# Optimization experiments

Measured on AMD Instinct MI355X. Metric: run time of the kernel, lower is better.

The kernel has to match this reference:

```python
import jax, jax.numpy as jnp
import numpy as np


def _binarize_ste(w):
    # forward: sign(w) in {-1, +1}; backward: identity (straight-through)
    wb = jnp.where(w >= 0, 1.0, -1.0).astype(w.dtype)
    return w + jax.lax.stop_gradient(wb - w)


def setup_inputs() -> dict:
    key = jax.random.key(0)
    k1, k2 = jax.random.split(key)
    IN, OUT, N = 2048, 2048, 8192
    x = jax.random.normal(k1, (N, IN), dtype=jnp.float32)
    # kaiming_uniform-like init: U(-bound, bound), bound = sqrt(6/in)*? (gain sqrt(5) default in torch)
    bound = float(np.sqrt(6.0 / IN))
    weight = jax.random.uniform(k2, (OUT, IN), dtype=jnp.float32, minval=-bound, maxval=bound)
    bias = jnp.zeros((OUT,), dtype=jnp.float32)
    return {"x": x, "weight": weight, "bias": bias}


def reference(x, weight, bias):
    w_binary = _binarize_ste(weight)  # [out, in], values in {-1, +1}
    # F.linear: x @ W^T + b
    return jnp.einsum('ni,oi->no', x, w_binary) + bias
```

## Files before the change

kernel.cpp:

```cpp
#include <hip/hip_runtime.h>
#include <stdint.h>


typedef __bf16 bf16x8 __attribute__((ext_vector_type(8)));
typedef float f32x4 __attribute__((ext_vector_type(4)));

typedef const __attribute__((address_space(1))) void* gas_ptr;
typedef __attribute__((address_space(3))) void* lds_ptr;

__device__ __forceinline__ unsigned short f2bf_rne(float f) {
    unsigned int u = __builtin_bit_cast(unsigned int, f);
    u += 0x7fffu + ((u >> 16) & 1u);
    return (unsigned short)(u >> 16);
}

__global__ __launch_bounds__(256) void prep_kernel(
    const float* __restrict__ x, const float* __restrict__ w,
    unsigned short* __restrict__ xb, unsigned short* __restrict__ wb,
    int nx8, int nxB, int nw4)
{
    const int b = blockIdx.x;
    if (b < nxB) {
        int i = b * 256 + threadIdx.x;
        if (i >= nx8) return;
        const float4* p = reinterpret_cast<const float4*>(x + (size_t)i * 8);
        float4 f0 = p[0], f1 = p[1];
        union { unsigned short s[8]; uint4 v; } o;
        o.s[0] = f2bf_rne(f0.x); o.s[1] = f2bf_rne(f0.y);
        o.s[2] = f2bf_rne(f0.z); o.s[3] = f2bf_rne(f0.w);
        o.s[4] = f2bf_rne(f1.x); o.s[5] = f2bf_rne(f1.y);
        o.s[6] = f2bf_rne(f1.z); o.s[7] = f2bf_rne(f1.w);
        *reinterpret_cast<uint4*>(xb + (size_t)i * 8) = o.v;
    } else {
        int i = (b - nxB) * 256 + threadIdx.x;
        if (i >= nw4) return;
        float4 f = reinterpret_cast<const float4*>(w)[i];
        union { unsigned short s[4]; uint2 v; } o;
        o.s[0] = (f.x >= 0.f) ? 0x3F80u : 0xBF80u;
        o.s[1] = (f.y >= 0.f) ? 0x3F80u : 0xBF80u;
        o.s[2] = (f.z >= 0.f) ? 0x3F80u : 0xBF80u;
        o.s[3] = (f.w >= 0.f) ? 0x3F80u : 0xBF80u;
        reinterpret_cast<uint2*>(wb)[i] = o.v;
    }
}

#define WAITLGKM0 asm volatile("s_waitcnt lgkmcnt(0)")
#define WAITLGKM8 asm volatile("s_waitcnt lgkmcnt(8)")
#define WAITVM0   asm volatile("s_waitcnt vmcnt(0)")
#define SBAR      __builtin_amdgcn_s_barrier()
#define SCHEDB    __builtin_amdgcn_sched_barrier(0)

__global__ __launch_bounds__(512, 2) void gemm_bin_kernel(
    const unsigned short* __restrict__ A,
    const unsigned short* __restrict__ B,
    const float* __restrict__ bias,
    float* __restrict__ C,
    int M, int N, int K)
{
    __shared__ __align__(16) unsigned char smem_raw[131072];
    unsigned short* const sm = (unsigned short*)smem_raw;

    const int tid  = threadIdx.x;
    const int lane = tid & 63;
    const int wave = tid >> 6;
    const int wm   = wave >> 2;
    const int wn   = wave & 3;
    const int bm   = blockIdx.y;
    const int bn   = blockIdx.x;

    const unsigned short* __restrict__ Agb = A + (size_t)(bm * 256) * K;
    const unsigned short* __restrict__ Bgb = B + (size_t)(bn * 256) * K;

    const int r15 = lane & 15;
    const int kc  = lane >> 4;
    const int sw  = ((r15 >> 2) & 1) << 1;

    const int baseA0 = wm * 8192 + r15 * 64 + ((kc    ) ^ sw) * 8;
    const int baseA1 = wm * 8192 + r15 * 64 + ((kc + 4) ^ sw) * 8;
    const int bBq    = 16384 + (wn >> 1) * 8192 + (wn & 1) * 4096 + r15 * 64;
    const int baseB0 = bBq + ((kc    ) ^ sw) * 8;
    const int baseB1 = bBq + ((kc + 4) ^ sw) * 8;

    int gsoff[2], ldoff[2];
#pragma unroll
    for (int j = 0; j < 2; ++j) {
        const int g  = j * 512 + tid;
        const int rl = g >> 3;
        const int c  = (g & 7) ^ (((rl >> 2) & 1) << 1);
        gsoff[j] = rl * K + c * 8;
        ldoff[j] = g * 8;
    }

    const int colb = bn * 256 + wn * 64;
    float bv[4];
#pragma unroll
    for (int nf = 0; nf < 4; ++nf) {
        bv[nf] = bias[colb + nf * 16 + r15];
        asm volatile("" :: "v"(bv[nf]));
    }

    f32x4 acc[8][4];
#pragma unroll
    for (int m = 0; m < 8; ++m)
#pragma unroll
        for (int n = 0; n < 4; ++n)
#pragma unroll
            for (int r = 0; r < 4; ++r) acc[m][n][r] = 0.f;

    bf16x8 bfr[4][2];

    auto stage2 = [&](const unsigned short* gsrc, unsigned short* dst) {
#pragma unroll
        for (int j = 0; j < 2; ++j)
            __builtin_amdgcn_global_load_lds((gas_ptr)(gsrc + gsoff[j]),
                                             (lds_ptr)(dst + ldoff[j]), 16, 0, 0);
    };

    const int KT = K >> 6;

    stage2(Agb,                   sm);
    stage2(Agb + (size_t)128 * K, sm + 8192);
    stage2(Bgb,                   sm + 16384);
    stage2(Bgb + (size_t)128 * K, sm + 24576);
    WAITVM0;
    SBAR;
    SCHEDB;
    asm volatile("" ::: "memory");

    for (int T = 0; T < KT; ++T) {
        const unsigned short* bb = sm + (T & 1) * 32768;
        unsigned short* nb = sm + ((T + 1) & 1) * 32768;
        const int pf = (T + 1 < KT);
        const unsigned short* gaN = Agb + (size_t)(T + 1) * 64;
        const unsigned short* gbN = Bgb + (size_t)(T + 1) * 64;

#pragma unroll
        for (int mh = 0; mh < 4; ++mh) {
            if (mh == 0) {
#pragma unroll
                for (int nf = 0; nf < 4; ++nf) {
                    bfr[nf][0] = *reinterpret_cast<const bf16x8*>(bb + baseB0 + nf * 1024);
                    bfr[nf][1] = *reinterpret_cast<const bf16x8*>(bb + baseB1 + nf * 1024);
                }
            }
            bf16x8 af[2][2];
#pragma unroll
            for (int mi = 0; mi < 2; ++mi) {
                af[mi][0] = *reinterpret_cast<const bf16x8*>(bb + baseA0 + (mh * 2 + mi) * 1024);
                af[mi][1] = *reinterpret_cast<const bf16x8*>(bb + baseA1 + (mh * 2 + mi) * 1024);
            }
            if (mh == 0 && pf) {
                stage2(gaN,                   nb);
                stage2(gaN + (size_t)128 * K, nb + 8192);
            }
            if (mh == 1 && pf) {
                stage2(gbN,                   nb + 16384);
                stage2(gbN + (size_t)128 * K, nb + 24576);
            }
            if (mh == 0) WAITLGKM8;
            SBAR;
            WAITLGKM0;
            __builtin_amdgcn_s_setprio(1);
#pragma unroll
            for (int kk = 0; kk < 2; ++kk)
#pragma unroll
                for (int mi = 0; mi < 2; ++mi)
#pragma unroll
                    for (int nf = 0; nf < 4; ++nf)
                        acc[mh * 2 + mi][nf] = __builtin_amdgcn_mfma_f32_16x16x32_bf16(
                            af[mi][kk], bfr[nf][kk], acc[mh * 2 + mi][nf], 0, 0, 0);
            __builtin_amdgcn_s_setprio(0);
            if (mh == 3) WAITVM0;
            SBAR;
            if (mh == 3) {
                SCHEDB;
                asm volatile("" ::: "memory");
            }
        }
    }

    const int row0 = bm * 256 + wm * 128 + kc * 4;
#pragma unroll
    for (int mf = 0; mf < 8; ++mf)
#pragma unroll
        for (int nf = 0; nf < 4; ++nf) {
            float* cp = C + (size_t)(row0 + mf * 16) * N + colb + nf * 16 + r15;
#pragma unroll
            for (int r = 0; r < 4; ++r)
                cp[(size_t)r * N] = acc[mf][nf][r] + bv[nf];
        }
}

extern "C" void kernel_launch(void* const* d_in, const int* in_sizes, int n_in,
                              void* d_out, int out_size, void* d_ws, size_t ws_size,
                              hipStream_t stream) {
    const float* x    = (const float*)d_in[0];
    const float* w    = (const float*)d_in[1];
    const float* bias = (const float*)d_in[2];
    float* out = (float*)d_out;

    const int K = 2048;
    const int N = in_sizes[2];
    const int M = in_sizes[0] / K;

    unsigned short* xb = (unsigned short*)d_ws;
    unsigned short* wb = xb + (size_t)M * K;

    const int nx8 = (M * K) / 8;
    const int nw4 = (N * K) / 4;
    const int nxB = (nx8 + 255) / 256;
    const int nwB = (nw4 + 255) / 256;
    prep_kernel<<<nxB + nwB, 256, 0, stream>>>(x, w, xb, wb, nx8, nxB, nw4);

    dim3 grid(N / 256, M / 256);
    gemm_bin_kernel<<<grid, 512, 0, stream>>>(xb, wb, bias, out, M, N, K);
}
```

Before: 191.3 us.

## Pack binarized weights into bitmasks and expand to bf16 in registers

The prep kernel now packs the signs of the weights into one bit each, laid out per 64-wide K tile. The GEMM loads these bits straight into registers and expands them into bf16 ±1 MFMA operands, so weight tiles no longer pass through LDS. The A tile moves to a 3-slot LDS ring with deeper prefetch, using split vmcnt waits. This cuts weight bandwidth and LDS traffic and lowers LDS use, but adds ALU work for the bit expansion and uncoalesced 8-byte global loads per lane.

```diff
diff --git a/kernel.cpp b/kernel.cpp
--- a/kernel.cpp
+++ b/kernel.cpp
@@ -16,8 +16,8 @@
 
 __global__ __launch_bounds__(256) void prep_kernel(
     const float* __restrict__ x, const float* __restrict__ w,
-    unsigned short* __restrict__ xb, unsigned short* __restrict__ wb,
-    int nx8, int nxB, int nw4)
+    unsigned short* __restrict__ xb, unsigned char* __restrict__ wbits,
+    int nx8, int nxB, int nw8, int K)
 {
     const int b = blockIdx.x;
     if (b < nxB) {
@@ -33,31 +33,39 @@
         *reinterpret_cast<uint4*>(xb + (size_t)i * 8) = o.v;
     } else {
         int i = (b - nxB) * 256 + threadIdx.x;
-        if (i >= nw4) return;
-        float4 f = reinterpret_cast<const float4*>(w)[i];
-        union { unsigned short s[4]; uint2 v; } o;
-        o.s[0] = (f.x >= 0.f) ? 0x3F80u : 0xBF80u;
-        o.s[1] = (f.y >= 0.f) ? 0x3F80u : 0xBF80u;
-        o.s[2] = (f.z >= 0.f) ? 0x3F80u : 0xBF80u;
-        o.s[3] = (f.w >= 0.f) ? 0x3F80u : 0xBF80u;
-        reinterpret_cast<uint2*>(wb)[i] = o.v;
+        if (i >= nw8) return;
+        const int kt = i >> 14;
+        const int n  = (i >> 3) & 2047;
+        const int kb = i & 7;
+        const float4* p = reinterpret_cast<const float4*>(
+            w + (size_t)n * K + kt * 64 + kb * 8);
+        float4 f0 = p[0], f1 = p[1];
+        unsigned bt = 0;
+        bt |= (f0.x >= 0.f) ? 0u : 1u;
+        bt |= (f0.y >= 0.f) ? 0u : 2u;
+        bt |= (f0.z >= 0.f) ? 0u : 4u;
+        bt |= (f0.w >= 0.f) ? 0u : 8u;
+        bt |= (f1.x >= 0.f) ? 0u : 16u;
+        bt |= (f1.y >= 0.f) ? 0u : 32u;
+        bt |= (f1.z >= 0.f) ? 0u : 64u;
+        bt |= (f1.w >= 0.f) ? 0u : 128u;
+        wbits[i] = (unsigned char)bt;
     }
 }
 
 #define WAITLGKM0 asm volatile("s_waitcnt lgkmcnt(0)")
-#define WAITLGKM8 asm volatile("s_waitcnt lgkmcnt(8)")
-#define WAITVM0   asm volatile("s_waitcnt vmcnt(0)")
+#define WAITVM8   asm volatile("s_waitcnt vmcnt(8)")
+#define WAITVM4   asm volatile("s_waitcnt vmcnt(4)")
 #define SBAR      __builtin_amdgcn_s_barrier()
-#define SCHEDB    __builtin_amdgcn_sched_barrier(0)
 
 __global__ __launch_bounds__(512, 2) void gemm_bin_kernel(
     const unsigned short* __restrict__ A,
-    const unsigned short* __restrict__ B,
+    const unsigned char*  __restrict__ Wb,
     const float* __restrict__ bias,
     float* __restrict__ C,
     int M, int N, int K)
 {
-    __shared__ __align__(16) unsigned char smem_raw[131072];
+    __shared__ __align__(16) unsigned char smem_raw[98304];
     unsigned short* const sm = (unsigned short*)smem_raw;
 
     const int tid  = threadIdx.x;
@@ -69,7 +77,6 @@
     const int bn   = blockIdx.x;
 
     const unsigned short* __restrict__ Agb = A + (size_t)(bm * 256) * K;
-    const unsigned short* __restrict__ Bgb = B + (size_t)(bn * 256) * K;
 
     const int r15 = lane & 15;
     const int kc  = lane >> 4;
@@ -77,13 +84,10 @@
 
     const int baseA0 = wm * 8192 + r15 * 64 + ((kc    ) ^ sw) * 8;
     const int baseA1 = wm * 8192 + r15 * 64 + ((kc + 4) ^ sw) * 8;
-    const int bBq    = 16384 + (wn >> 1) * 8192 + (wn & 1) * 4096 + r15 * 64;
-    const int baseB0 = bBq + ((kc    ) ^ sw) * 8;
-    const int baseB1 = bBq + ((kc + 4) ^ sw) * 8;
-
-    int gsoff[2], ldoff[2];
-#pragma unroll
-    for (int j = 0; j < 2; ++j) {
+
+    int gsoff[4], ldoff[4];
+#pragma unroll
+    for (int j = 0; j < 4; ++j) {
         const int g  = j * 512 + tid;
         const int rl = g >> 3;
         const int c  = (g & 7) ^ (((rl >> 2) & 1) << 1);
@@ -107,57 +111,63 @@
 #pragma unroll
             for (int r = 0; r < 4; ++r) acc[m][n][r] = 0.f;
 
+    uint2 bitsCur[4], bitsNxt[4];
     bf16x8 bfr[4][2];
-
-    auto stage2 = [&](const unsigned short* gsrc, unsigned short* dst) {
-#pragma unroll
-        for (int j = 0; j < 2; ++j)
-            __builtin_amdgcn_global_load_lds((gas_ptr)(gsrc + gsoff[j]),
-                                             (lds_ptr)(dst + ldoff[j]), 16, 0, 0);
+    const int shb = kc * 8;
+
+    auto loadbits = [&](int kt, uint2* dst) {
+        const unsigned char* base = Wb + (size_t)kt * ((size_t)N * 8);
+#pragma unroll
+        for (int nf = 0; nf < 4; ++nf)
+            dst[nf] = *reinterpret_cast<const uint2*>(
+                base + (size_t)(colb + nf * 16 + r15) * 8);
     };
+    auto stageA = [&](int T, int slot) {
+        unsigned short* d = sm + slot * 16384;
+        const unsigned short* g = Agb + (size_t)T * 64;
+#pragma unroll
+        for (int j = 0; j < 4; ++j)
+            __builtin_amdgcn_global_load_lds((gas_ptr)(g + gsoff[j]),
+                                             (lds_ptr)(d + ldoff[j]), 16, 0, 0);
+    };
+    auto expand = [&]() {
+#pragma unroll
+        for (int nf = 0; nf < 4; ++nf)
+#pragma unroll
+            for (int kk = 0; kk < 2; ++kk) {
+                unsigned w32 = kk ? bitsCur[nf].y : bitsCur[nf].x;
+                unsigned bbits = (w32 >> shb) & 0xffu;
+                union { unsigned u[4]; bf16x8 v; } o;
+                o.u[0] = 0x3F803F80u | ((bbits &   1u) << 15) | ((bbits &   2u) << 30);
+                o.u[1] = 0x3F803F80u | ((bbits &   4u) << 13) | ((bbits &   8u) << 28);
+                o.u[2] = 0x3F803F80u | ((bbits &  16u) << 11) | ((bbits &  32u) << 26);
+                o.u[3] = 0x3F803F80u | ((bbits &  64u) <<  9) | ((bbits & 128u) << 24);
+                bfr[nf][kk] = o.v;
+            }
+    };
 
     const int KT = K >> 6;
 
-    stage2(Agb,                   sm);
-    stage2(Agb + (size_t)128 * K, sm + 8192);
-    stage2(Bgb,                   sm + 16384);
-    stage2(Bgb + (size_t)128 * K, sm + 24576);
-    WAITVM0;
+    loadbits(0, bitsCur);
+    stageA(0, 0);
+    stageA(1, 1);
+    WAITVM4;
     SBAR;
-    SCHEDB;
-    asm volatile("" ::: "memory");
-
+
+    int sc = 0, sp = 2;
     for (int T = 0; T < KT; ++T) {
-        const unsigned short* bb = sm + (T & 1) * 32768;
-        unsigned short* nb = sm + ((T + 1) & 1) * 32768;
-        const int pf = (T + 1 < KT);
-        const unsigned short* gaN = Agb + (size_t)(T + 1) * 64;
-        const unsigned short* gbN = Bgb + (size_t)(T + 1) * 64;
-
+        const unsigned short* bb = sm + sc * 16384;
 #pragma unroll
         for (int mh = 0; mh < 4; ++mh) {
-            if (mh == 0) {
-#pragma unroll
-                for (int nf = 0; nf < 4; ++nf) {
-                    bfr[nf][0] = *reinterpret_cast<const bf16x8*>(bb + baseB0 + nf * 1024);
-                    bfr[nf][1] = *reinterpret_cast<const bf16x8*>(bb + baseB1 + nf * 1024);
-                }
-            }
+            if (mh == 0) expand();
             bf16x8 af[2][2];
 #pragma unroll
             for (int mi = 0; mi < 2; ++mi) {
                 af[mi][0] = *reinterpret_cast<const bf16x8*>(bb + baseA0 + (mh * 2 + mi) * 1024);
                 af[mi][1] = *reinterpret_cast<const bf16x8*>(bb + baseA1 + (mh * 2 + mi) * 1024);
             }
-            if (mh == 0 && pf) {
-                stage2(gaN,                   nb);
-                stage2(gaN + (size_t)128 * K, nb + 8192);
-            }
-            if (mh == 1 && pf) {
-                stage2(gbN,                   nb + 16384);
-                stage2(gbN + (size_t)128 * K, nb + 24576);
-            }
-            if (mh == 0) WAITLGKM8;
+            if (mh == 0 && T + 1 < KT) loadbits(T + 1, bitsNxt);
+            if (mh == 1 && T + 2 < KT) stageA(T + 2, sp);
             SBAR;
             WAITLGKM0;
             __builtin_amdgcn_s_setprio(1);
@@ -170,13 +180,16 @@
                         acc[mh * 2 + mi][nf] = __builtin_amdgcn_mfma_f32_16x16x32_bf16(
                             af[mi][kk], bfr[nf][kk], acc[mh * 2 + mi][nf], 0, 0, 0);
             __builtin_amdgcn_s_setprio(0);
-            if (mh == 3) WAITVM0;
+            if (mh == 3) {
+                if (T < KT - 2)       { WAITVM8; }
+                else if (T == KT - 2) { WAITVM4; }
+            }
             SBAR;
-            if (mh == 3) {
-                SCHEDB;
-                asm volatile("" ::: "memory");
-            }
         }
+#pragma unroll
+        for (int nf = 0; nf < 4; ++nf) bitsCur[nf] = bitsNxt[nf];
+        sc = (sc == 2) ? 0 : sc + 1;
+        sp = (sp == 2) ? 0 : sp + 1;
     }
 
     const int row0 = bm * 256 + wm * 128 + kc * 4;
@@ -204,14 +217,14 @@
     const int M = in_sizes[0] / K;
 
     unsigned short* xb = (unsigned short*)d_ws;
-    unsigned short* wb = xb + (size_t)M * K;
+    unsigned char* wbits = (unsigned char*)(xb + (size_t)M * K);
 
     const int nx8 = (M * K) / 8;
-    const int nw4 = (N * K) / 4;
+    const int nw8 = (N * K) / 8;
     const int nxB = (nx8 + 255) / 256;
-    const int nwB = (nw4 + 255) / 256;
-    prep_kernel<<<nxB + nwB, 256, 0, stream>>>(x, w, xb, wb, nx8, nxB, nw4);
+    const int nwB = (nw8 + 255) / 256;
+    prep_kernel<<<nxB + nwB, 256, 0, stream>>>(x, w, xb, wbits, nx8, nxB, nw8, K);
 
     dim3 grid(N / 256, M / 256);
-    gemm_bin_kernel<<<grid, 512, 0, stream>>>(xb, wb, bias, out, M, N, K);
-}
+    gemm_bin_kernel<<<grid, 512, 0, stream>>>(xb, wbits, bias, out, M, N, K);
+}
```

Measured after the change: 207.1 us. 8.2% more time.

## Restructure GEMM main loop into 4-stage K=32 pipeline with prefetch depth two

Applied to the files above, without the earlier changes.

Replaces the double-buffered K=64 tile loop with a four-slot ring of K=32 stages, prefetching two stages ahead and waiting with vmcnt(4) so global loads stay in flight across iterations. The LDS layout changes to 32-element rows with a new XOR swizzle, and A/B staging is split across two half-steps of MFMA work. This aims to hide global-to-LDS latency better, at the cost of more barriers per K element and possible new LDS bank conflicts.

```diff
diff --git a/kernel.cpp b/kernel.cpp
--- a/kernel.cpp
+++ b/kernel.cpp
@@ -45,10 +45,9 @@
 }
 
 #define WAITLGKM0 asm volatile("s_waitcnt lgkmcnt(0)")
-#define WAITLGKM8 asm volatile("s_waitcnt lgkmcnt(8)")
+#define WAITVM4   asm volatile("s_waitcnt vmcnt(4)")
 #define WAITVM0   asm volatile("s_waitcnt vmcnt(0)")
 #define SBAR      __builtin_amdgcn_s_barrier()
-#define SCHEDB    __builtin_amdgcn_sched_barrier(0)
 
 __global__ __launch_bounds__(512, 2) void gemm_bin_kernel(
     const unsigned short* __restrict__ A,
@@ -73,20 +72,27 @@
 
     const int r15 = lane & 15;
     const int kc  = lane >> 4;
-    const int sw  = ((r15 >> 2) & 1) << 1;
-
-    const int baseA0 = wm * 8192 + r15 * 64 + ((kc    ) ^ sw) * 8;
-    const int baseA1 = wm * 8192 + r15 * 64 + ((kc + 4) ^ sw) * 8;
-    const int bBq    = 16384 + (wn >> 1) * 8192 + (wn & 1) * 4096 + r15 * 64;
-    const int baseB0 = bBq + ((kc    ) ^ sw) * 8;
-    const int baseB1 = bBq + ((kc + 4) ^ sw) * 8;
+
+    int baseA[2][4], baseB[4];
+#pragma unroll
+    for (int mh = 0; mh < 2; ++mh)
+#pragma unroll
+        for (int mf = 0; mf < 4; ++mf) {
+            const int row = wm * 128 + mh * 64 + mf * 16 + r15;
+            baseA[mh][mf] = row * 32 + (kc ^ ((row >> 1) & 3)) * 8;
+        }
+#pragma unroll
+    for (int nf = 0; nf < 4; ++nf) {
+        const int row = wn * 64 + nf * 16 + r15;
+        baseB[nf] = 8192 + row * 32 + (kc ^ ((row >> 1) & 3)) * 8;
+    }
 
     int gsoff[2], ldoff[2];
 #pragma unroll
     for (int j = 0; j < 2; ++j) {
         const int g  = j * 512 + tid;
-        const int rl = g >> 3;
-        const int c  = (g & 7) ^ (((rl >> 2) & 1) << 1);
+        const int rl = g >> 2;
+        const int c  = (g & 3) ^ ((rl >> 1) & 3);
         gsoff[j] = rl * K + c * 8;
         ldoff[j] = g * 8;
     }
@@ -107,76 +113,65 @@
 #pragma unroll
             for (int r = 0; r < 4; ++r) acc[m][n][r] = 0.f;
 
-    bf16x8 bfr[4][2];
-
-    auto stage2 = [&](const unsigned short* gsrc, unsigned short* dst) {
+    auto stageP = [&](const unsigned short* g, unsigned short* d) {
 #pragma unroll
         for (int j = 0; j < 2; ++j)
-            __builtin_amdgcn_global_load_lds((gas_ptr)(gsrc + gsoff[j]),
-                                             (lds_ptr)(dst + ldoff[j]), 16, 0, 0);
+            __builtin_amdgcn_global_load_lds((gas_ptr)(g + gsoff[j]),
+                                             (lds_ptr)(d + ldoff[j]), 16, 0, 0);
     };
 
-    const int KT = K >> 6;
-
-    stage2(Agb,                   sm);
-    stage2(Agb + (size_t)128 * K, sm + 8192);
-    stage2(Bgb,                   sm + 16384);
-    stage2(Bgb + (size_t)128 * K, sm + 24576);
-    WAITVM0;
+    const int NS = K >> 5;
+
+    stageP(Agb,      sm);
+    stageP(Bgb,      sm + 8192);
+    stageP(Agb + 32, sm + 16384);
+    stageP(Bgb + 32, sm + 16384 + 8192);
+    WAITVM4;
     SBAR;
-    SCHEDB;
-    asm volatile("" ::: "memory");
-
-    for (int T = 0; T < KT; ++T) {
-        const unsigned short* bb = sm + (T & 1) * 32768;
-        unsigned short* nb = sm + ((T + 1) & 1) * 32768;
-        const int pf = (T + 1 < KT);
-        const unsigned short* gaN = Agb + (size_t)(T + 1) * 64;
-        const unsigned short* gbN = Bgb + (size_t)(T + 1) * 64;
-
-#pragma unroll
-        for (int mh = 0; mh < 4; ++mh) {
-            if (mh == 0) {
-#pragma unroll
-                for (int nf = 0; nf < 4; ++nf) {
-                    bfr[nf][0] = *reinterpret_cast<const bf16x8*>(bb + baseB0 + nf * 1024);
-                    bfr[nf][1] = *reinterpret_cast<const bf16x8*>(bb + baseB1 + nf * 1024);
-                }
-            }
-            bf16x8 af[2][2];
-#pragma unroll
-            for (int mi = 0; mi < 2; ++mi) {
-                af[mi][0] = *reinterpret_cast<const bf16x8*>(bb + baseA0 + (mh * 2 + mi) * 1024);
-                af[mi][1] = *reinterpret_cast<const bf16x8*>(bb + baseA1 + (mh * 2 + mi) * 1024);
-            }
-            if (mh == 0 && pf) {
-                stage2(gaN,                   nb);
-                stage2(gaN + (size_t)128 * K, nb + 8192);
-            }
-            if (mh == 1 && pf) {
-                stage2(gbN,                   nb + 16384);
-                stage2(gbN + (size_t)128 * K, nb + 24576);
-            }
-            if (mh == 0) WAITLGKM8;
-            SBAR;
-            WAITLGKM0;
-            __builtin_amdgcn_s_setprio(1);
-#pragma unroll
-            for (int kk = 0; kk < 2; ++kk)
-#pragma unroll
-                for (int mi = 0; mi < 2; ++mi)
-#pragma unroll
-                    for (int nf = 0; nf < 4; ++nf)
-                        acc[mh * 2 + mi][nf] = __builtin_amdgcn_mfma_f32_16x16x32_bf16(
-                            af[mi][kk], bfr[nf][kk], acc[mh * 2 + mi][nf], 0, 0, 0);
-            __builtin_amdgcn_s_setprio(0);
-            if (mh == 3) WAITVM0;
-            SBAR;
-            if (mh == 3) {
-                SCHEDB;
-                asm volatile("" ::: "memory");
-            }
-        }
+
+#pragma unroll 4
+    for (int s = 0; s < NS; ++s) {
+        const unsigned short* us = sm + (s & 3) * 16384;
+        unsigned short* sp = sm + ((s + 2) & 3) * 16384;
+        const int pf = (s + 2 < NS);
+
+        bf16x8 bfr[4], afr[4];
+#pragma unroll
+        for (int nf = 0; nf < 4; ++nf)
+            bfr[nf] = *reinterpret_cast<const bf16x8*>(us + baseB[nf]);
+#pragma unroll
+        for (int mf = 0; mf < 4; ++mf)
+            afr[mf] = *reinterpret_cast<const bf16x8*>(us + baseA[0][mf]);
+        if (pf) stageP(Agb + (size_t)(s + 2) * 32, sp);
+        SBAR;
+        WAITLGKM0;
+        __builtin_amdgcn_s_setprio(1);
+#pragma unroll
+        for (int mf = 0; mf < 4; ++mf)
+#pragma unroll
+            for (int nf = 0; nf < 4; ++nf)
+                acc[mf][nf] = __builtin_amdgcn_mfma_f32_16x16x32_bf16(
+                    afr[mf], bfr[nf], acc[mf][nf], 0, 0, 0);
+        __builtin_amdgcn_s_setprio(0);
+        SBAR;
+
+#pragma unroll
+        for (int mf = 0; mf < 4; ++mf)
+            afr[mf] = *reinterpret_cast<const bf16x8*>(us + baseA[1][mf]);
+        if (pf) stageP(Bgb + (size_t)(s + 2) * 32, sp + 8192);
+        SBAR;
+        WAITLGKM0;
+        __builtin_amdgcn_s_setprio(1);
+#pragma unroll
+        for (int mf = 0; mf < 4; ++mf)
+#pragma unroll
+            for (int nf = 0; nf < 4; ++nf)
+                acc[4 + mf][nf] = __builtin_amdgcn_mfma_f32_16x16x32_bf16(
+                    afr[mf], bfr[nf], acc[4 + mf][nf], 0, 0, 0);
+        __builtin_amdgcn_s_setprio(0);
+        if (pf)                 { WAITVM4; }
+        else if (s + 1 < NS)    { WAITVM0; }
+        SBAR;
     }
 
     const int row0 = bm * 256 + wm * 128 + kc * 4;
```

Result: no change. 189.6 us (-0.9%).

## Load B fragments straight from global into registers, stage only A in LDS

Applied to the files above, without the earlier changes.

The GEMM now streams only the A tile through double-buffered LDS. Each wave loads its B (binarized weight) MFMA fragments directly from global memory into registers, double-buffered across K tiles. This halves the LDS footprint and drops the per-subtile barriers and lgkm waits in favor of one barrier per tile, and the A swizzle is changed to a new XOR pattern. The prep kernel also converts x four floats per thread instead of eight. The trade-off is that the B global loads are small strided per-lane reads that are not shared across waves, and they add register pressure from two B fragment sets.

```diff
diff --git a/kernel.cpp b/kernel.cpp
--- a/kernel.cpp
+++ b/kernel.cpp
@@ -17,20 +17,17 @@
 __global__ __launch_bounds__(256) void prep_kernel(
     const float* __restrict__ x, const float* __restrict__ w,
     unsigned short* __restrict__ xb, unsigned short* __restrict__ wb,
-    int nx8, int nxB, int nw4)
+    int nx4, int nxB, int nw4)
 {
     const int b = blockIdx.x;
     if (b < nxB) {
         int i = b * 256 + threadIdx.x;
-        if (i >= nx8) return;
-        const float4* p = reinterpret_cast<const float4*>(x + (size_t)i * 8);
-        float4 f0 = p[0], f1 = p[1];
-        union { unsigned short s[8]; uint4 v; } o;
-        o.s[0] = f2bf_rne(f0.x); o.s[1] = f2bf_rne(f0.y);
-        o.s[2] = f2bf_rne(f0.z); o.s[3] = f2bf_rne(f0.w);
-        o.s[4] = f2bf_rne(f1.x); o.s[5] = f2bf_rne(f1.y);
-        o.s[6] = f2bf_rne(f1.z); o.s[7] = f2bf_rne(f1.w);
-        *reinterpret_cast<uint4*>(xb + (size_t)i * 8) = o.v;
+        if (i >= nx4) return;
+        float4 f = reinterpret_cast<const float4*>(x)[i];
+        union { unsigned short s[4]; uint2 v; } o;
+        o.s[0] = f2bf_rne(f.x); o.s[1] = f2bf_rne(f.y);
+        o.s[2] = f2bf_rne(f.z); o.s[3] = f2bf_rne(f.w);
+        reinterpret_cast<uint2*>(xb)[i] = o.v;
     } else {
         int i = (b - nxB) * 256 + threadIdx.x;
         if (i >= nw4) return;
@@ -44,8 +41,6 @@
     }
 }
 
-#define WAITLGKM0 asm volatile("s_waitcnt lgkmcnt(0)")
-#define WAITLGKM8 asm volatile("s_waitcnt lgkmcnt(8)")
 #define WAITVM0   asm volatile("s_waitcnt vmcnt(0)")
 #define SBAR      __builtin_amdgcn_s_barrier()
 #define SCHEDB    __builtin_amdgcn_sched_barrier(0)
@@ -57,7 +52,7 @@
     float* __restrict__ C,
     int M, int N, int K)
 {
-    __shared__ __align__(16) unsigned char smem_raw[131072];
+    __shared__ __align__(16) unsigned char smem_raw[65536];
     unsigned short* const sm = (unsigned short*)smem_raw;
 
     const int tid  = threadIdx.x;
@@ -69,25 +64,22 @@
     const int bn   = blockIdx.x;
 
     const unsigned short* __restrict__ Agb = A + (size_t)(bm * 256) * K;
-    const unsigned short* __restrict__ Bgb = B + (size_t)(bn * 256) * K;
 
     const int r15 = lane & 15;
     const int kc  = lane >> 4;
-    const int sw  = ((r15 >> 2) & 1) << 1;
-
-    const int baseA0 = wm * 8192 + r15 * 64 + ((kc    ) ^ sw) * 8;
-    const int baseA1 = wm * 8192 + r15 * 64 + ((kc + 4) ^ sw) * 8;
-    const int bBq    = 16384 + (wn >> 1) * 8192 + (wn & 1) * 4096 + r15 * 64;
-    const int baseB0 = bBq + ((kc    ) ^ sw) * 8;
-    const int baseB1 = bBq + ((kc + 4) ^ sw) * 8;
+    const int msk = ((r15 & 1) << 2) | ((r15 >> 1) & 3);
+
+    const int offA0 = (wm * 128 + r15) * 64 + ((kc    ) ^ msk) * 8;
+    const int offA1 = (wm * 128 + r15) * 64 + ((kc + 4) ^ msk) * 8;
 
     int gsoff[2], ldoff[2];
 #pragma unroll
     for (int j = 0; j < 2; ++j) {
         const int g  = j * 512 + tid;
         const int rl = g >> 3;
-        const int c  = (g & 7) ^ (((rl >> 2) & 1) << 1);
-        gsoff[j] = rl * K + c * 8;
+        const int pc = g & 7;
+        const int ml = ((rl & 1) << 2) | ((rl >> 1) & 3);
+        gsoff[j] = rl * K + (pc ^ ml) * 8;
         ldoff[j] = g * 8;
     }
 
@@ -99,6 +91,11 @@
         asm volatile("" :: "v"(bv[nf]));
     }
 
+    const unsigned short* Bg[4];
+#pragma unroll
+    for (int nf = 0; nf < 4; ++nf)
+        Bg[nf] = B + (size_t)(colb + nf * 16 + r15) * K + kc * 8;
+
     f32x4 acc[8][4];
 #pragma unroll
     for (int m = 0; m < 8; ++m)
@@ -107,76 +104,68 @@
 #pragma unroll
             for (int r = 0; r < 4; ++r) acc[m][n][r] = 0.f;
 
-    bf16x8 bfr[4][2];
-
-    auto stage2 = [&](const unsigned short* gsrc, unsigned short* dst) {
+    bf16x8 b0[4][2], b1[4][2];
+
+    auto stageH = [&](int T, int h, unsigned short* buf) {
+        const unsigned short* g = Agb + (size_t)(h * 128) * K + (size_t)T * 64;
+        unsigned short* d = buf + h * 8192;
 #pragma unroll
         for (int j = 0; j < 2; ++j)
-            __builtin_amdgcn_global_load_lds((gas_ptr)(gsrc + gsoff[j]),
-                                             (lds_ptr)(dst + ldoff[j]), 16, 0, 0);
+            __builtin_amdgcn_global_load_lds((gas_ptr)(g + gsoff[j]),
+                                             (lds_ptr)(d + ldoff[j]), 16, 0, 0);
     };
+    auto loadB = [&](int T, bf16x8 (&dst)[4][2]) {
+#pragma unroll
+        for (int nf = 0; nf < 4; ++nf)
+#pragma unroll
+            for (int kk = 0; kk < 2; ++kk)
+                dst[nf][kk] = *reinterpret_cast<const bf16x8*>(
+                    Bg[nf] + (size_t)T * 64 + kk * 32);
+    };
+
+    auto tileBody = [&](int T, const unsigned short* bb, unsigned short* nb,
+                        bf16x8 (&bc)[4][2], bf16x8 (&bn_)[4][2], bool pf) {
+        if (pf) {
+            stageH(T + 1, 0, nb);
+            stageH(T + 1, 1, nb);
+            loadB(T + 1, bn_);
+        }
+#pragma unroll
+        for (int p = 0; p < 4; ++p) {
+            bf16x8 af[2][2];
+#pragma unroll
+            for (int mi = 0; mi < 2; ++mi) {
+                af[mi][0] = *reinterpret_cast<const bf16x8*>(bb + offA0 + (p * 2 + mi) * 1024);
+                af[mi][1] = *reinterpret_cast<const bf16x8*>(bb + offA1 + (p * 2 + mi) * 1024);
+            }
+            __builtin_amdgcn_s_setprio(1);
+#pragma unroll
+            for (int kk = 0; kk < 2; ++kk)
+#pragma unroll
+                for (int mi = 0; mi < 2; ++mi)
+#pragma unroll
+                    for (int nf = 0; nf < 4; ++nf)
+                        acc[p * 2 + mi][nf] = __builtin_amdgcn_mfma_f32_16x16x32_bf16(
+                            af[mi][kk], bc[nf][kk], acc[p * 2 + mi][nf], 0, 0, 0);
+            __builtin_amdgcn_s_setprio(0);
+        }
+        SCHEDB;
+        WAITVM0;
+        SBAR;
+    };
 
     const int KT = K >> 6;
 
-    stage2(Agb,                   sm);
-    stage2(Agb + (size_t)128 * K, sm + 8192);
-    stage2(Bgb,                   sm + 16384);
-    stage2(Bgb + (size_t)128 * K, sm + 24576);
+    stageH(0, 0, sm);
+    stageH(0, 1, sm);
+    loadB(0, b0);
+    SCHEDB;
     WAITVM0;
     SBAR;
-    SCHEDB;
-    asm volatile("" ::: "memory");
-
-    for (int T = 0; T < KT; ++T) {
-        const unsigned short* bb = sm + (T & 1) * 32768;
-        unsigned short* nb = sm + ((T + 1) & 1) * 32768;
-        const int pf = (T + 1 < KT);
-        const unsigned short* gaN = Agb + (size_t)(T + 1) * 64;
-        const unsigned short* gbN = Bgb + (size_t)(T + 1) * 64;
-
-#pragma unroll
-        for (int mh = 0; mh < 4; ++mh) {
-            if (mh == 0) {
-#pragma unroll
-                for (int nf = 0; nf < 4; ++nf) {
-                    bfr[nf][0] = *reinterpret_cast<const bf16x8*>(bb + baseB0 + nf * 1024);
-                    bfr[nf][1] = *reinterpret_cast<const bf16x8*>(bb + baseB1 + nf * 1024);
-                }
-            }
-            bf16x8 af[2][2];
-#pragma unroll
-            for (int mi = 0; mi < 2; ++mi) {
-                af[mi][0] = *reinterpret_cast<const bf16x8*>(bb + baseA0 + (mh * 2 + mi) * 1024);
-                af[mi][1] = *reinterpret_cast<const bf16x8*>(bb + baseA1 + (mh * 2 + mi) * 1024);
-            }
-            if (mh == 0 && pf) {
-                stage2(gaN,                   nb);
-                stage2(gaN + (size_t)128 * K, nb + 8192);
-            }
-            if (mh == 1 && pf) {
-                stage2(gbN,                   nb + 16384);
-                stage2(gbN + (size_t)128 * K, nb + 24576);
-            }
-            if (mh == 0) WAITLGKM8;
-            SBAR;
-            WAITLGKM0;
-            __builtin_amdgcn_s_setprio(1);
-#pragma unroll
-            for (int kk = 0; kk < 2; ++kk)
-#pragma unroll
-                for (int mi = 0; mi < 2; ++mi)
-#pragma unroll
-                    for (int nf = 0; nf < 4; ++nf)
-                        acc[mh * 2 + mi][nf] = __builtin_amdgcn_mfma_f32_16x16x32_bf16(
-                            af[mi][kk], bfr[nf][kk], acc[mh * 2 + mi][nf], 0, 0, 0);
-            __builtin_amdgcn_s_setprio(0);
-            if (mh == 3) WAITVM0;
-            SBAR;
-            if (mh == 3) {
-                SCHEDB;
-                asm volatile("" ::: "memory");
-            }
-        }
+
+    for (int T2 = 0; T2 < KT; T2 += 2) {
+        tileBody(T2,     sm,         sm + 16384, b0, b1, true);
+        tileBody(T2 + 1, sm + 16384, sm,         b1, b0, T2 + 2 < KT);
     }
 
     const int row0 = bm * 256 + wm * 128 + kc * 4;
@@ -206,11 +195,11 @@
     unsigned short* xb = (unsigned short*)d_ws;
     unsigned short* wb = xb + (size_t)M * K;
 
-    const int nx8 = (M * K) / 8;
+    const int nx4 = (M * K) / 4;
     const int nw4 = (N * K) / 4;
-    const int nxB = (nx8 + 255) / 256;
+    const int nxB = (nx4 + 255) / 256;
     const int nwB = (nw4 + 255) / 256;
-    prep_kernel<<<nxB + nwB, 256, 0, stream>>>(x, w, xb, wb, nx8, nxB, nw4);
+    prep_kernel<<<nxB + nwB, 256, 0, stream>>>(x, w, xb, wb, nx4, nxB, nw4);
 
     dim3 grid(N / 256, M / 256);
     gemm_bin_kernel<<<grid, 512, 0, stream>>>(xb, wb, bias, out, M, N, K);
```

Measured after the change: 234.3 us. 22.5% more time.
